# Performance work log

Hardware: AMD Instinct MI355X
Metric: run time of the kernel (lower is better)

## Reference

```python
import jax, jax.numpy as jnp
import numpy as np

# ---- config constants (cfg) ----
AA, LP, Tc = 1.0, 1.0, 1.0
OMEGA_PHI, ALPHA_PHI, Lc = 1.0, 0.01, 1.0
CSE, CLE = 0.5, 0.00574
AC_PRE_SCALE = 1.0
AC1 = 2 * AA * LP * Tc
AC2 = LP * OMEGA_PHI * Tc
AC3 = LP * ALPHA_PHI * Tc / Lc**2

N, HID, NLAYERS, EMB = 65536, 128, 4, 64  # 2*EMB == HID


def setup_inputs() -> dict:
    key = jax.random.key(0)
    ks = jax.random.split(key, 6)
    x = jax.random.uniform(ks[0], (N, 2), dtype=jnp.float32)
    t = jax.random.uniform(ks[1], (N, 1), dtype=jnp.float32)
    B = jax.random.normal(ks[2], (3, EMB), dtype=jnp.float32)  # fourier features
    Wh = jax.random.normal(ks[3], (NLAYERS, HID, HID), dtype=jnp.float32) / np.sqrt(HID)
    bh = jnp.zeros((NLAYERS, HID), dtype=jnp.float32)
    Wout = jax.random.normal(ks[4], (HID, 2), dtype=jnp.float32) / np.sqrt(HID)
    bout = jnp.zeros((2,), dtype=jnp.float32)
    return {"x": x, "t": t, "B": B, "Wh": Wh, "bh": bh, "Wout": Wout, "bout": bout}


def reference(x, t, B, Wh, bh, Wout, bout):
    mirror = jnp.array([-1.0, 1.0], dtype=x.dtype)

    def mlp(xx, tt):  # xx:(2,), tt:(1,) -> (2,)
        z = jnp.concatenate([xx, tt])              # (3,)
        f = 2 * jnp.pi * (z @ B)                   # (EMB,)
        h = jnp.concatenate([jnp.sin(f), jnp.cos(f)])  # (HID,)
        def layer(h, wb):
            W, b = wb
            return jnp.tanh(h @ W + b), None
        h, _ = jax.lax.scan(layer, h, (Wh, bh))
        return h @ Wout + bout

    def net_u(xx, tt):  # hard-constrained (phi, c), symmetrized in x
        def hard_cons(xx_):
            phi, cl = jnp.tanh(mlp(xx_, tt)) / 2 + 0.5
            cl = cl * (1 - CSE + CLE)
            c = (CSE - CLE) * (-2 * phi**3 + 3 * phi**2) + cl
            return jnp.stack([phi, c])
        return (hard_cons(xx) + hard_cons(xx * mirror)) / 2

    def net_ac_point(xx, tt):  # Allen-Cahn residual at one collocation point
        phi, c = net_u(xx, tt)
        h_phi = -2 * phi**3 + 3 * phi**2
        dh_dphi = -6 * phi**2 + 6 * phi
        dg_dphi = 4 * phi**3 - 6 * phi**2 + 2 * phi
        dphi_dt = jax.jacrev(lambda t_: net_u(xx, t_)[0])(tt)          # (1,)
        hess = jax.hessian(lambda x_: net_u(x_, tt)[0])(xx)            # (2,2)
        nabla2phi = jnp.trace(hess)
        ac = (dphi_dt.squeeze()
              - AC1 * (c - h_phi * (CSE - CLE) - CLE) * (CSE - CLE) * dh_dphi
              + AC2 * dg_dphi
              - AC3 * nabla2phi)
        return ac / AC_PRE_SCALE

    return jax.vmap(net_ac_point)(x, t)  # (N,) PDE residuals
```

## Files before the change

### kernel.cpp

```cpp
#include <hip/hip_runtime.h>
#include <math.h>

#define PTS_PER_BLOCK 9
#define NPTS_PER_WAVE 3
#define WAVES_PER_BLOCK 3

typedef _Float16 h8 __attribute__((ext_vector_type(8)));
typedef _Float16 h2 __attribute__((ext_vector_type(2)));
typedef __fp16   fp16x2 __attribute__((ext_vector_type(2)));
typedef float    f4 __attribute__((ext_vector_type(4)));
typedef unsigned int uint32;

#define CSE_C 0.5f
#define CLE_C 0.00574f
#define DCOEF (CSE_C - CLE_C)
#define KCOEF (1.0f - CSE_C + CLE_C)

__device__ __forceinline__ float tanh_fast(float xx) {
    float e = __expf(2.0f * xx);
    float r = __builtin_amdgcn_rcpf(e + 1.0f);
    return fmaf(-2.0f, r, 1.0f);
}
__device__ __forceinline__ unsigned short f2h(float a) {
    union { _Float16 h; unsigned short u; } ua; ua.h = (_Float16)a; return ua.u;
}
__device__ __forceinline__ h2 pkrtz(float a, float b) {
    union { fp16x2 f; h2 h; } x; x.f = __builtin_amdgcn_cvt_pkrtz(a, b); return x.h;
}
__device__ __forceinline__ uint32 pk2h(float a, float b) {
    union { h2 h; uint32 u; } x; x.h = pkrtz(a, b); return x.u;
}
__device__ __forceinline__ h8 h8_from4(uint32 a, uint32 b, uint32 c, uint32 d) {
    union { uint32 u[4]; h8 v; } x; x.u[0] = a; x.u[1] = b; x.u[2] = c; x.u[3] = d;
    return x.v;
}

extern "C" __global__ __launch_bounds__(256)
void pinn_prep(const float* __restrict__ Wh, uint32* __restrict__ Wp)
{
    int gid  = blockIdx.x * 256 + threadIdx.x;
    int d    = gid & 3;
    int lane = (gid >> 2) & 63;
    int kt   = (gid >> 8) & 3;
    int jo   = (gid >> 10) & 7;
    int L    = gid >> 13;
    int j    = kt * 32 + (lane >> 4) * 8 + 2 * d;
    int jout = jo * 16 + (lane & 15);
    float w0 = Wh[(L * 128 + j) * 128 + jout];
    float w1 = Wh[(L * 128 + j + 1) * 128 + jout];
    Wp[gid] = pk2h(w0, w1);
}

extern "C" __global__ __launch_bounds__(192, 4)
void pinn_mfma(const float* __restrict__ x, const float* __restrict__ t,
               const float* __restrict__ B, const uint32* __restrict__ Wp,
               const float* __restrict__ bh, const float* __restrict__ Wout,
               const float* __restrict__ bout, float* __restrict__ out, int npts)
{
    __shared__ __align__(16) unsigned short H[WAVES_PER_BLOCK][32][136];

    const int tid  = threadIdx.x;
    const int lane = tid & 63;
    const int wv   = tid >> 6;
    const int c    = lane & 15;
    const int g    = lane >> 4;
    const int base_pt = blockIdx.x * PTS_PER_BLOCK + wv * NPTS_PER_WAVE;

    unsigned short* Hb = &H[wv][0][0];

    {
        const float TWO_PI = 6.28318530717958647692f;
        float b0 = TWO_PI * B[lane];
        float b1 = TWO_PI * B[64 + lane];
        float b2 = TWO_PI * B[128 + lane];
        float bsq = fmaf(b0, b0, b1 * b1);
        #pragma unroll
        for (int b = 0; b < 6; ++b) {
            int pl = b >> 1, mir = b & 1;
            int pt = base_pt + pl; if (pt > npts - 1) pt = npts - 1;
            float x0 = x[2 * pt], x1 = x[2 * pt + 1], tt = t[pt];
            if (mir) x0 = -x0;
            float f = fmaf(x0, b0, fmaf(x1, b1, tt * b2));
            float sf, cf; __sincosf(f, &sf, &cf);
            int rs = (b < 3) ? 5 * b : 16 + 5 * (b - 3);
            Hb[(rs + 0) * 136 + lane] = f2h(sf);
            Hb[(rs + 1) * 136 + lane] = f2h(cf * b2);
            Hb[(rs + 2) * 136 + lane] = f2h(cf * b0);
            Hb[(rs + 3) * 136 + lane] = f2h(cf * b1);
            Hb[(rs + 4) * 136 + lane] = f2h(-sf * bsq);
            Hb[(rs + 0) * 136 + 64 + lane] = f2h(cf);
            Hb[(rs + 1) * 136 + 64 + lane] = f2h(-sf * b2);
            Hb[(rs + 2) * 136 + 64 + lane] = f2h(-sf * b0);
            Hb[(rs + 3) * 136 + 64 + lane] = f2h(-sf * b1);
            Hb[(rs + 4) * 136 + 64 + lane] = f2h(-cf * bsq);
        }
    }
    asm volatile("s_waitcnt lgkmcnt(0)" ::: "memory");

    for (int L = 0; L < 4; ++L) {
        h8 bf[2][4];
        #pragma unroll
        for (int ct = 0; ct < 2; ++ct)
            #pragma unroll
            for (int kt = 0; kt < 4; ++kt)
                bf[ct][kt] = *(const h8*)&Hb[(ct * 16 + c) * 136 + kt * 32 + g * 8];

        const uint4* WL = (const uint4*)Wp + (size_t)L * 2048;

        uint4 wt[2][4];
        #pragma unroll
        for (int kt = 0; kt < 4; ++kt) wt[0][kt] = WL[kt * 64 + lane];

        #pragma unroll
        for (int jo = 0; jo < 8; ++jo) {
            const int cur = jo & 1, nxt = cur ^ 1;
            if (jo < 7) {
                #pragma unroll
                for (int kt = 0; kt < 4; ++kt)
                    wt[nxt][kt] = WL[((jo + 1) * 4 + kt) * 64 + lane];
            }
            f4 a0 = {0.f, 0.f, 0.f, 0.f}, a1 = {0.f, 0.f, 0.f, 0.f};
            #pragma unroll
            for (int kt = 0; kt < 4; ++kt) {
                union { uint4 u; h8 v; } af;
                af.u = wt[cur][kt];
                a0 = __builtin_amdgcn_mfma_f32_16x16x32_f16(af.v, bf[0][kt], a0, 0, 0, 0);
                a1 = __builtin_amdgcn_mfma_f32_16x16x32_f16(af.v, bf[1][kt], a1, 0, 0, 0);
            }
            union { h2 h[2]; uint2 u; } w0, w1;
            w0.h[0] = pkrtz(a0[0], a0[1]); w0.h[1] = pkrtz(a0[2], a0[3]);
            w1.h[0] = pkrtz(a1[0], a1[1]); w1.h[1] = pkrtz(a1[2], a1[3]);
            *(uint2*)&Hb[(0  + c) * 136 + jo * 16 + g * 4] = w0.u;
            *(uint2*)&Hb[(16 + c) * 136 + jo * 16 + g * 4] = w1.u;
        }
        asm volatile("s_waitcnt lgkmcnt(0)" ::: "memory");

        {
            const int jb = 2 * lane;
            const float2 bj = *(const float2*)&bh[L * 128 + jb];
            const h2 bias2 = pkrtz(bj.x, bj.y);
            const h2 m2 = {(_Float16)(-2.0f), (_Float16)(-2.0f)};
            #pragma unroll
            for (int b = 0; b < 6; ++b) {
                int rs = (b < 3) ? 5 * b : 16 + 5 * (b - 3);
                h2 vp = *(const h2*)&Hb[(rs + 0) * 136 + jb];
                h2 tp = *(const h2*)&Hb[(rs + 1) * 136 + jb];
                h2 pp = *(const h2*)&Hb[(rs + 2) * 136 + jb];
                h2 qp = *(const h2*)&Hb[(rs + 3) * 136 + jb];
                h2 Lp = *(const h2*)&Hb[(rs + 4) * 136 + jb];
                vp = vp + bias2;
                float y0 = tanh_fast((float)vp[0]);
                float y1 = tanh_fast((float)vp[1]);
                h2 yp = pkrtz(y0, y1);
                h2 sp = pkrtz(fmaf(-y0, y0, 1.f), fmaf(-y1, y1, 1.f));
                h2 qq = __builtin_elementwise_fma(pp, pp, qp * qp);
                h2 Ln = sp * __builtin_elementwise_fma(yp * m2, qq, Lp);
                *(h2*)&Hb[(rs + 0) * 136 + jb] = yp;
                *(h2*)&Hb[(rs + 1) * 136 + jb] = sp * tp;
                *(h2*)&Hb[(rs + 2) * 136 + jb] = sp * pp;
                *(h2*)&Hb[(rs + 3) * 136 + jb] = sp * qp;
                *(h2*)&Hb[(rs + 4) * 136 + jb] = Ln;
            }
        }
        asm volatile("s_waitcnt lgkmcnt(0)" ::: "memory");
    }

    {
        h8 afo[4];
        const int   mc  = c & 1;
        const float sel = (c < 2) ? 1.0f : 0.0f;
        #pragma unroll
        for (int kt = 0; kt < 4; ++kt) {
            uint32 u[4];
            #pragma unroll
            for (int d = 0; d < 4; ++d) {
                int k = kt * 32 + g * 8 + 2 * d;
                float w0 = Wout[k * 2 + mc] * sel;
                float w1 = Wout[(k + 1) * 2 + mc] * sel;
                u[d] = pk2h(w0, w1);
            }
            afo[kt] = h8_from4(u[0], u[1], u[2], u[3]);
        }
        h8 bfo[2][4];
        #pragma unroll
        for (int ct = 0; ct < 2; ++ct)
            #pragma unroll
            for (int kt = 0; kt < 4; ++kt)
                bfo[ct][kt] = *(const h8*)&Hb[(ct * 16 + c) * 136 + kt * 32 + g * 8];

        f4 ac0 = {0.f, 0.f, 0.f, 0.f}, ac1 = {0.f, 0.f, 0.f, 0.f};
        #pragma unroll
        for (int kt = 0; kt < 4; ++kt) {
            ac0 = __builtin_amdgcn_mfma_f32_16x16x32_f16(afo[kt], bfo[0][kt], ac0, 0, 0, 0);
            ac1 = __builtin_amdgcn_mfma_f32_16x16x32_f16(afo[kt], bfo[1][kt], ac1, 0, 0, 0);
        }
        float* S = (float*)Hb;
        if (g == 0) {
            f4 pack = {ac0[0], ac0[1], ac1[0], ac1[1]};
            *(f4*)&S[c * 4] = pack;
        }
        asm volatile("s_waitcnt lgkmcnt(0)" ::: "memory");

        if (lane < 3) {
            int pt = base_pt + lane;
            if (pt < npts) {
                float bo0 = bout[0], bo1 = bout[1];
                float ph = 0.f, cv = 0.f, ptd = 0.f, lp = 0.f;
                #pragma unroll
                for (int br = 0; br < 2; ++br) {
                    int b  = 2 * lane + br;
                    int ct = (b < 3) ? 0 : 1;
                    int cc = ((b < 3) ? b : b - 3) * 5;
                    float o0v = S[(cc + 0) * 4 + 2 * ct] + bo0;
                    float o0t = S[(cc + 1) * 4 + 2 * ct];
                    float o0p = S[(cc + 2) * 4 + 2 * ct];
                    float o0q = S[(cc + 3) * 4 + 2 * ct];
                    float o0L = S[(cc + 4) * 4 + 2 * ct];
                    float o1v = S[(cc + 0) * 4 + 2 * ct + 1] + bo1;
                    float T = tanh_fast(o0v);
                    float p = fmaf(0.5f, T, 0.5f);
                    float s = 0.5f * fmaf(-T, T, 1.f);
                    float lap = s * o0L - 2.f * T * s * fmaf(o0p, o0p, o0q * o0q);
                    float cl = KCOEF * fmaf(0.5f, tanh_fast(o1v), 0.5f);
                    float cb = fmaf(DCOEF, (-2.f * p + 3.f) * p * p, cl);
                    ph  += 0.5f * p;
                    cv  += 0.5f * cb;
                    ptd += 0.5f * s * o0t;
                    lp  += 0.5f * lap;
                }
                float hph = (-2.f * ph + 3.f) * ph * ph;
                float dh  = 6.f * ph * (1.f - ph);
                float dg  = ((4.f * ph - 6.f) * ph + 2.f) * ph;
                float ac  = ptd
                          - 2.f * ((cv - hph * DCOEF - CLE_C) * DCOEF) * dh
                          + dg
                          - 0.01f * lp;
                out[pt] = ac;
            }
        }
    }
}

extern "C" void kernel_launch(void* const* d_in, const int* in_sizes, int n_in,
                              void* d_out, int out_size, void* d_ws, size_t ws_size,
                              hipStream_t stream) {
    const float* x    = (const float*)d_in[0];
    const float* t    = (const float*)d_in[1];
    const float* B    = (const float*)d_in[2];
    const float* Wh   = (const float*)d_in[3];
    const float* bh   = (const float*)d_in[4];
    const float* Wout = (const float*)d_in[5];
    const float* bout = (const float*)d_in[6];
    float* out = (float*)d_out;
    uint32* Wp = (uint32*)d_ws;

    const int npts = in_sizes[0] / 2;
    hipLaunchKernelGGL(pinn_prep, dim3(128), dim3(256), 0, stream, Wh, Wp);
    const int nb = (npts + PTS_PER_BLOCK - 1) / PTS_PER_BLOCK;
    hipLaunchKernelGGL(pinn_mfma, dim3(nb), dim3(192), 0, stream,
                       x, t, B, Wp, bh, Wout, bout, out, npts);
}
```

Before: 137.5 us.

## Swizzle LDS activation layout, deepen weight prefetch, use native sin/cos

Rewrites the per-wave shared-memory activation tile to use an XOR-swizzled byte layout keyed on row parity, with the MFMA B-fragment read split into two 8-byte loads, to cut LDS bank conflicts in the MFMA read, result write and elementwise passes. Weight-tile prefetch grows from double to triple buffering so global loads are issued two j-blocks ahead. The Fourier feature step now reduces the argument to [0,1) with floor and calls the hardware sin/cos intrinsics, sharing the x1/t part between the two mirrored branches. Costs are more registers for the third weight buffer and more address arithmetic, which may lower occupancy.

```diff
diff --git a/kernel.cpp b/kernel.cpp
--- a/kernel.cpp
+++ b/kernel.cpp
@@ -29,6 +29,11 @@
 }
 __device__ __forceinline__ uint32 pk2h(float a, float b) {
     union { h2 h; uint32 u; } x; x.h = pkrtz(a, b); return x.u;
+}
+__device__ __forceinline__ h8 h8_from2x2(uint2 lo, uint2 hi) {
+    union { uint32 u[4]; h8 v; } x;
+    x.u[0] = lo.x; x.u[1] = lo.y; x.u[2] = hi.x; x.u[3] = hi.y;
+    return x.v;
 }
 __device__ __forceinline__ h8 h8_from4(uint32 a, uint32 b, uint32 c, uint32 d) {
     union { uint32 u[4]; h8 v; } x; x.u[0] = a; x.u[1] = b; x.u[2] = c; x.u[3] = d;
@@ -66,33 +71,47 @@
     const int g    = lane >> 4;
     const int base_pt = blockIdx.x * PTS_PER_BLOCK + wv * NPTS_PER_WAVE;
 
-    unsigned short* Hb = &H[wv][0][0];
+    unsigned char* Hc = (unsigned char*)&H[wv][0][0];
+
+    const int par   = c & 1;
+    const int e0    = lane * 2;
+    const int e1    = e0 ^ 8;
+    const int pb0   = lane * 4;
+    const int pb1   = pb0 ^ 8;
+    const int wb0   = c * 272 + ((g * 8) ^ (par << 3));
+    const int fb_lo = c * 272 + g * 16 + (par << 3);
+    const int fb_hi = fb_lo ^ 8;
 
     {
         const float TWO_PI = 6.28318530717958647692f;
-        float b0 = TWO_PI * B[lane];
-        float b1 = TWO_PI * B[64 + lane];
-        float b2 = TWO_PI * B[128 + lane];
-        float bsq = fmaf(b0, b0, b1 * b1);
-        #pragma unroll
-        for (int b = 0; b < 6; ++b) {
-            int pl = b >> 1, mir = b & 1;
+        const float Br0 = B[lane], Br1 = B[64 + lane], Br2 = B[128 + lane];
+        const float b0 = TWO_PI * Br0, b1 = TWO_PI * Br1, b2 = TWO_PI * Br2;
+        const float bsq = fmaf(b0, b0, b1 * b1);
+        #pragma unroll
+        for (int pl = 0; pl < 3; ++pl) {
             int pt = base_pt + pl; if (pt > npts - 1) pt = npts - 1;
-            float x0 = x[2 * pt], x1 = x[2 * pt + 1], tt = t[pt];
-            if (mir) x0 = -x0;
-            float f = fmaf(x0, b0, fmaf(x1, b1, tt * b2));
-            float sf, cf; __sincosf(f, &sf, &cf);
-            int rs = (b < 3) ? 5 * b : 16 + 5 * (b - 3);
-            Hb[(rs + 0) * 136 + lane] = f2h(sf);
-            Hb[(rs + 1) * 136 + lane] = f2h(cf * b2);
-            Hb[(rs + 2) * 136 + lane] = f2h(cf * b0);
-            Hb[(rs + 3) * 136 + lane] = f2h(cf * b1);
-            Hb[(rs + 4) * 136 + lane] = f2h(-sf * bsq);
-            Hb[(rs + 0) * 136 + 64 + lane] = f2h(cf);
-            Hb[(rs + 1) * 136 + 64 + lane] = f2h(-sf * b2);
-            Hb[(rs + 2) * 136 + 64 + lane] = f2h(-sf * b0);
-            Hb[(rs + 3) * 136 + 64 + lane] = f2h(-sf * b1);
-            Hb[(rs + 4) * 136 + 64 + lane] = f2h(-cf * bsq);
+            const float2 xx = *(const float2*)&x[2 * pt];
+            const float tt = t[pt];
+            const float uc = fmaf(xx.y, Br1, tt * Br2);
+            const float ux = xx.x * Br0;
+            #pragma unroll
+            for (int mir = 0; mir < 2; ++mir) {
+                float u = mir ? (uc - ux) : (uc + ux);
+                float r = u - floorf(u);
+                float sf = __builtin_amdgcn_sinf(r);
+                float cf = __builtin_amdgcn_cosf(r);
+                const int b  = pl * 2 + mir;
+                const int rs = (b < 3) ? 5 * b : 16 + 5 * (b - 3);
+                const float sv[5] = { sf,  cf * b2,  cf * b0,  cf * b1, -sf * bsq };
+                const float cv[5] = { cf, -sf * b2, -sf * b0, -sf * b1, -cf * bsq };
+                #pragma unroll
+                for (int ch = 0; ch < 5; ++ch) {
+                    const int row = rs + ch;
+                    const int eb  = (row & 1) ? e1 : e0;
+                    *(unsigned short*)(Hc + eb + row * 272)       = f2h(sv[ch]);
+                    *(unsigned short*)(Hc + eb + row * 272 + 128) = f2h(cv[ch]);
+                }
+            }
         }
     }
     asm volatile("s_waitcnt lgkmcnt(0)" ::: "memory");
@@ -102,52 +121,56 @@
         #pragma unroll
         for (int ct = 0; ct < 2; ++ct)
             #pragma unroll
-            for (int kt = 0; kt < 4; ++kt)
-                bf[ct][kt] = *(const h8*)&Hb[(ct * 16 + c) * 136 + kt * 32 + g * 8];
+            for (int kt = 0; kt < 4; ++kt) {
+                uint2 lo = *(const uint2*)(Hc + fb_lo + ct * 4352 + kt * 64);
+                uint2 hi = *(const uint2*)(Hc + fb_hi + ct * 4352 + kt * 64);
+                bf[ct][kt] = h8_from2x2(lo, hi);
+            }
 
         const uint4* WL = (const uint4*)Wp + (size_t)L * 2048;
 
-        uint4 wt[2][4];
+        uint4 wt[3][4];
         #pragma unroll
         for (int kt = 0; kt < 4; ++kt) wt[0][kt] = WL[kt * 64 + lane];
+        #pragma unroll
+        for (int kt = 0; kt < 4; ++kt) wt[1][kt] = WL[(4 + kt) * 64 + lane];
 
         #pragma unroll
         for (int jo = 0; jo < 8; ++jo) {
-            const int cur = jo & 1, nxt = cur ^ 1;
-            if (jo < 7) {
+            if (jo < 6) {
                 #pragma unroll
                 for (int kt = 0; kt < 4; ++kt)
-                    wt[nxt][kt] = WL[((jo + 1) * 4 + kt) * 64 + lane];
+                    wt[(jo + 2) % 3][kt] = WL[((jo + 2) * 4 + kt) * 64 + lane];
             }
             f4 a0 = {0.f, 0.f, 0.f, 0.f}, a1 = {0.f, 0.f, 0.f, 0.f};
             #pragma unroll
             for (int kt = 0; kt < 4; ++kt) {
                 union { uint4 u; h8 v; } af;
-                af.u = wt[cur][kt];
+                af.u = wt[jo % 3][kt];
                 a0 = __builtin_amdgcn_mfma_f32_16x16x32_f16(af.v, bf[0][kt], a0, 0, 0, 0);
                 a1 = __builtin_amdgcn_mfma_f32_16x16x32_f16(af.v, bf[1][kt], a1, 0, 0, 0);
             }
             union { h2 h[2]; uint2 u; } w0, w1;
             w0.h[0] = pkrtz(a0[0], a0[1]); w0.h[1] = pkrtz(a0[2], a0[3]);
             w1.h[0] = pkrtz(a1[0], a1[1]); w1.h[1] = pkrtz(a1[2], a1[3]);
-            *(uint2*)&Hb[(0  + c) * 136 + jo * 16 + g * 4] = w0.u;
-            *(uint2*)&Hb[(16 + c) * 136 + jo * 16 + g * 4] = w1.u;
+            *(uint2*)(Hc + wb0 + jo * 32)        = w0.u;
+            *(uint2*)(Hc + wb0 + 4352 + jo * 32) = w1.u;
         }
         asm volatile("s_waitcnt lgkmcnt(0)" ::: "memory");
 
         {
-            const int jb = 2 * lane;
-            const float2 bj = *(const float2*)&bh[L * 128 + jb];
+            const float2 bj = *(const float2*)&bh[L * 128 + 2 * lane];
             const h2 bias2 = pkrtz(bj.x, bj.y);
             const h2 m2 = {(_Float16)(-2.0f), (_Float16)(-2.0f)};
             #pragma unroll
             for (int b = 0; b < 6; ++b) {
-                int rs = (b < 3) ? 5 * b : 16 + 5 * (b - 3);
-                h2 vp = *(const h2*)&Hb[(rs + 0) * 136 + jb];
-                h2 tp = *(const h2*)&Hb[(rs + 1) * 136 + jb];
-                h2 pp = *(const h2*)&Hb[(rs + 2) * 136 + jb];
-                h2 qp = *(const h2*)&Hb[(rs + 3) * 136 + jb];
-                h2 Lp = *(const h2*)&Hb[(rs + 4) * 136 + jb];
+                const int rs = (b < 3) ? 5 * b : 16 + 5 * (b - 3);
+                #define PB(k) (Hc + (((rs + (k)) & 1) ? pb1 : pb0) + (rs + (k)) * 272)
+                h2 vp = *(const h2*)PB(0);
+                h2 tp = *(const h2*)PB(1);
+                h2 pp = *(const h2*)PB(2);
+                h2 qp = *(const h2*)PB(3);
+                h2 Lp = *(const h2*)PB(4);
                 vp = vp + bias2;
                 float y0 = tanh_fast((float)vp[0]);
                 float y1 = tanh_fast((float)vp[1]);
@@ -155,11 +178,12 @@
                 h2 sp = pkrtz(fmaf(-y0, y0, 1.f), fmaf(-y1, y1, 1.f));
                 h2 qq = __builtin_elementwise_fma(pp, pp, qp * qp);
                 h2 Ln = sp * __builtin_elementwise_fma(yp * m2, qq, Lp);
-                *(h2*)&Hb[(rs + 0) * 136 + jb] = yp;
-                *(h2*)&Hb[(rs + 1) * 136 + jb] = sp * tp;
-                *(h2*)&Hb[(rs + 2) * 136 + jb] = sp * pp;
-                *(h2*)&Hb[(rs + 3) * 136 + jb] = sp * qp;
-                *(h2*)&Hb[(rs + 4) * 136 + jb] = Ln;
+                *(h2*)PB(0) = yp;
+                *(h2*)PB(1) = sp * tp;
+                *(h2*)PB(2) = sp * pp;
+                *(h2*)PB(3) = sp * qp;
+                *(h2*)PB(4) = Ln;
+                #undef PB
             }
         }
         asm volatile("s_waitcnt lgkmcnt(0)" ::: "memory");
@@ -185,8 +209,11 @@
         #pragma unroll
         for (int ct = 0; ct < 2; ++ct)
             #pragma unroll
-            for (int kt = 0; kt < 4; ++kt)
-                bfo[ct][kt] = *(const h8*)&Hb[(ct * 16 + c) * 136 + kt * 32 + g * 8];
+            for (int kt = 0; kt < 4; ++kt) {
+                uint2 lo = *(const uint2*)(Hc + fb_lo + ct * 4352 + kt * 64);
+                uint2 hi = *(const uint2*)(Hc + fb_hi + ct * 4352 + kt * 64);
+                bfo[ct][kt] = h8_from2x2(lo, hi);
+            }
 
         f4 ac0 = {0.f, 0.f, 0.f, 0.f}, ac1 = {0.f, 0.f, 0.f, 0.f};
         #pragma unroll
@@ -194,7 +221,7 @@
             ac0 = __builtin_amdgcn_mfma_f32_16x16x32_f16(afo[kt], bfo[0][kt], ac0, 0, 0, 0);
             ac1 = __builtin_amdgcn_mfma_f32_16x16x32_f16(afo[kt], bfo[1][kt], ac1, 0, 0, 0);
         }
-        float* S = (float*)Hb;
+        float* S = (float*)Hc;
         if (g == 0) {
             f4 pack = {ac0[0], ac0[1], ac1[0], ac1[1]};
             *(f4*)&S[c * 4] = pack;
```

New measurement: 145.4 us. 1.06x slower.

## Prefetch weights two tiles ahead across layers and use hardware sin/cos

Applied to the files above, without the earlier changes.

Weight tiles are now prefetched two steps ahead in a register ring that carries over layer boundaries, and the first layer's tiles are loaded before the Fourier feature setup so global latency hides behind that work. The Fourier phase is computed in revolutions and range-reduced with floor so the hardware sin/cos instructions can be used, and the two mirrored points share one x/t load. This targets global load stalls at each layer start and the cost of sincos. The trade-offs are higher register pressure and reliance on hardware trig accuracy after range reduction.

```diff
diff --git a/kernel.cpp b/kernel.cpp
--- a/kernel.cpp
+++ b/kernel.cpp
@@ -68,31 +68,46 @@
 
     unsigned short* Hb = &H[wv][0][0];
 
+    uint4 wt[2][4];
+    {
+        const uint4* W0 = (const uint4*)Wp;
+        #pragma unroll
+        for (int kt = 0; kt < 4; ++kt) wt[0][kt] = W0[kt * 64 + lane];
+        #pragma unroll
+        for (int kt = 0; kt < 4; ++kt) wt[1][kt] = W0[(4 + kt) * 64 + lane];
+    }
+
     {
         const float TWO_PI = 6.28318530717958647692f;
-        float b0 = TWO_PI * B[lane];
-        float b1 = TWO_PI * B[64 + lane];
-        float b2 = TWO_PI * B[128 + lane];
-        float bsq = fmaf(b0, b0, b1 * b1);
-        #pragma unroll
-        for (int b = 0; b < 6; ++b) {
-            int pl = b >> 1, mir = b & 1;
+        const float Br0 = B[lane], Br1 = B[64 + lane], Br2 = B[128 + lane];
+        const float b0 = TWO_PI * Br0, b1 = TWO_PI * Br1, b2 = TWO_PI * Br2;
+        const float bsq = fmaf(b0, b0, b1 * b1);
+        #pragma unroll
+        for (int pl = 0; pl < 3; ++pl) {
             int pt = base_pt + pl; if (pt > npts - 1) pt = npts - 1;
-            float x0 = x[2 * pt], x1 = x[2 * pt + 1], tt = t[pt];
-            if (mir) x0 = -x0;
-            float f = fmaf(x0, b0, fmaf(x1, b1, tt * b2));
-            float sf, cf; __sincosf(f, &sf, &cf);
-            int rs = (b < 3) ? 5 * b : 16 + 5 * (b - 3);
-            Hb[(rs + 0) * 136 + lane] = f2h(sf);
-            Hb[(rs + 1) * 136 + lane] = f2h(cf * b2);
-            Hb[(rs + 2) * 136 + lane] = f2h(cf * b0);
-            Hb[(rs + 3) * 136 + lane] = f2h(cf * b1);
-            Hb[(rs + 4) * 136 + lane] = f2h(-sf * bsq);
-            Hb[(rs + 0) * 136 + 64 + lane] = f2h(cf);
-            Hb[(rs + 1) * 136 + 64 + lane] = f2h(-sf * b2);
-            Hb[(rs + 2) * 136 + 64 + lane] = f2h(-sf * b0);
-            Hb[(rs + 3) * 136 + 64 + lane] = f2h(-sf * b1);
-            Hb[(rs + 4) * 136 + 64 + lane] = f2h(-cf * bsq);
+            const float2 xx = *(const float2*)&x[2 * pt];
+            const float tt = t[pt];
+            const float uc = fmaf(xx.y, Br1, tt * Br2);
+            const float ux = xx.x * Br0;
+            #pragma unroll
+            for (int mir = 0; mir < 2; ++mir) {
+                float u = mir ? (uc - ux) : (uc + ux);
+                float r = u - floorf(u);
+                float sf = __builtin_amdgcn_sinf(r);
+                float cf = __builtin_amdgcn_cosf(r);
+                const int b  = pl * 2 + mir;
+                const int rs = (b < 3) ? 5 * b : 16 + 5 * (b - 3);
+                Hb[(rs + 0) * 136 + lane] = f2h(sf);
+                Hb[(rs + 1) * 136 + lane] = f2h(cf * b2);
+                Hb[(rs + 2) * 136 + lane] = f2h(cf * b0);
+                Hb[(rs + 3) * 136 + lane] = f2h(cf * b1);
+                Hb[(rs + 4) * 136 + lane] = f2h(-sf * bsq);
+                Hb[(rs + 0) * 136 + 64 + lane] = f2h(cf);
+                Hb[(rs + 1) * 136 + 64 + lane] = f2h(-sf * b2);
+                Hb[(rs + 2) * 136 + 64 + lane] = f2h(-sf * b0);
+                Hb[(rs + 3) * 136 + 64 + lane] = f2h(-sf * b1);
+                Hb[(rs + 4) * 136 + 64 + lane] = f2h(-cf * bsq);
+            }
         }
     }
     asm volatile("s_waitcnt lgkmcnt(0)" ::: "memory");
@@ -106,19 +121,11 @@
                 bf[ct][kt] = *(const h8*)&Hb[(ct * 16 + c) * 136 + kt * 32 + g * 8];
 
         const uint4* WL = (const uint4*)Wp + (size_t)L * 2048;
-
-        uint4 wt[2][4];
-        #pragma unroll
-        for (int kt = 0; kt < 4; ++kt) wt[0][kt] = WL[kt * 64 + lane];
+        const uint4* WN = WL + 2048;
 
         #pragma unroll
         for (int jo = 0; jo < 8; ++jo) {
-            const int cur = jo & 1, nxt = cur ^ 1;
-            if (jo < 7) {
-                #pragma unroll
-                for (int kt = 0; kt < 4; ++kt)
-                    wt[nxt][kt] = WL[((jo + 1) * 4 + kt) * 64 + lane];
-            }
+            const int cur = jo & 1;
             f4 a0 = {0.f, 0.f, 0.f, 0.f}, a1 = {0.f, 0.f, 0.f, 0.f};
             #pragma unroll
             for (int kt = 0; kt < 4; ++kt) {
@@ -126,6 +133,15 @@
                 af.u = wt[cur][kt];
                 a0 = __builtin_amdgcn_mfma_f32_16x16x32_f16(af.v, bf[0][kt], a0, 0, 0, 0);
                 a1 = __builtin_amdgcn_mfma_f32_16x16x32_f16(af.v, bf[1][kt], a1, 0, 0, 0);
+            }
+            if (jo < 6) {
+                #pragma unroll
+                for (int kt = 0; kt < 4; ++kt)
+                    wt[cur][kt] = WL[((jo + 2) * 4 + kt) * 64 + lane];
+            } else if (L < 3) {
+                #pragma unroll
+                for (int kt = 0; kt < 4; ++kt)
+                    wt[cur][kt] = WN[((jo - 6) * 4 + kt) * 64 + lane];
             }
             union { h2 h[2]; uint2 u; } w0, w1;
             w0.h[0] = pkrtz(a0[0], a0[1]); w0.h[1] = pkrtz(a0[2], a0[3]);
```

New measurement: 138.5 us. No clear change (+0.7%).
